# Kernel optimization log

Measured on AMD Instinct MI355X. Metric: run time of the kernel, lower is better.

Reference implementation:

```python
import jax, jax.numpy as jnp
import numpy as np

B, T, N, IN_DIM, H = 8, 16, 1024, 2, 128
HEADS, HD = 8, 16            # HEADS*HD == H (DGL GATConv head-concat)
SNP, SEQ_OUT, DEG = 4, 12, 8
NT = SNP * N                 # nodes per HSTG graph
CKPNT = [4, 7, 10, 13, 16]   # _generate_checkpoints(4, 16)
LRELU = 0.2


def _build_edges():
    # HSTG: per-snapshot spatial edges (random deg-8 adjacency + self-loops)
    # plus identity temporal edges t -> t+1 (uni-direction, non-dense, sync).
    rng = np.random.default_rng(0)
    src, dst = [], []
    ar = np.arange(N)
    for t in range(SNP):
        off = t * N
        src.append(rng.integers(0, N, size=N * DEG) + off)
        dst.append(np.repeat(ar, DEG) + off)
        src.append(ar + off)   # self-loops (keep every dst non-empty)
        dst.append(ar + off)
    for t in range(SNP - 1):
        src.append(ar + t * N)
        dst.append(ar + (t + 1) * N)
    return (jnp.asarray(np.concatenate(src), dtype=jnp.int32),
            jnp.asarray(np.concatenate(dst), dtype=jnp.int32))


def setup_inputs() -> dict:
    key = jax.random.key(0)
    ks = jax.random.split(key, 16)
    edge_src, edge_dst = _build_edges()
    rn = lambda k, s, sc: jax.random.normal(k, s, dtype=jnp.float32) * sc
    return {
        'inputs': rn(ks[0], (B, T, N, IN_DIM), 1.0),
        'W_in': rn(ks[1], (IN_DIM, H), 0.5),
        'b_in': jnp.zeros((H,), jnp.float32),
        'spatial_emb': rn(ks[2], (N, H), 0.05),
        'temporal_emb': rn(ks[3], (N, T), 0.05),
        'gat_w0': rn(ks[4], (H, HEADS * HD), 0.1),
        'gat_al0': rn(ks[5], (HEADS, HD), 0.1),
        'gat_ar0': rn(ks[6], (HEADS, HD), 0.1),
        'gat_b0': jnp.zeros((HEADS * HD,), jnp.float32),
        'gat_w1': rn(ks[7], (H, HEADS * HD), 0.1),
        'gat_al1': rn(ks[8], (HEADS, HD), 0.1),
        'gat_ar1': rn(ks[9], (HEADS, HD), 0.1),
        'gat_b1': jnp.zeros((HEADS * HD,), jnp.float32),
        'agg_q': rn(ks[10], (N, H), 0.1),
        'w_out1': rn(ks[11], (1, SEQ_OUT), 0.5),
        'b_out1': jnp.zeros((SEQ_OUT,), jnp.float32),
        'w_out2': rn(ks[12], (H, 1), 0.1),
        'b_out2': jnp.zeros((1,), jnp.float32),
        'edge_src': edge_src,
        'edge_dst': edge_dst,
    }


def _gat_layer(x, W, a_l, a_r, b, src, dst, activate):
    # x: [NT, H] node features of one graph
    feat = (x @ W).reshape(NT, HEADS, HD)
    el = jnp.sum(feat * a_l, axis=-1)                 # [NT, HEADS]
    er = jnp.sum(feat * a_r, axis=-1)
    e = jax.nn.leaky_relu(el[src] + er[dst], LRELU)    # [E, HEADS]
    m = jax.ops.segment_max(e, dst, num_segments=NT)
    w = jnp.exp(e - m[dst])
    s = jax.ops.segment_sum(w, dst, num_segments=NT)
    alpha = w / s[dst]
    out = jax.ops.segment_sum(feat[src] * alpha[..., None], dst, num_segments=NT)
    out = out.reshape(NT, HEADS * HD) + b
    return jax.nn.elu(out) if activate else out


def reference(inputs, W_in, b_in, spatial_emb, temporal_emb,
              gat_w0, gat_al0, gat_ar0, gat_b0,
              gat_w1, gat_al1, gat_ar1, gat_b1,
              agg_q, w_out1, b_out1, w_out2, b_out2,
              edge_src, edge_dst):
    # input projection + spatial/temporal embeddings
    x = inputs @ W_in + b_in                           # [B,T,N,H]
    x = x + spatial_emb                                # broadcast [N,H]
    x = x + temporal_emb.T[None, :, :, None]           # add temb[n,t] at [b,t,n,h]

    def gat(xb):  # xb: [NT,H], one sample of the batched block-diagonal graph
        h = _gat_layer(xb, gat_w0, gat_al0, gat_ar0, gat_b0, edge_src, edge_dst, True)
        return _gat_layer(h, gat_w1, gat_al1, gat_ar1, gat_b1, edge_src, edge_dst, False)
    gat_b = jax.vmap(gat)

    last = None
    left = 0
    for idx, right in enumerate(CKPNT):
        fs = x[:, left:right]                          # [B, snp or snp-1, N, H]
        if idx != 0:
            fs = jnp.concatenate([last, fs], axis=1)   # [B, SNP, N, H]
        residual = fs
        h = gat_b(fs.reshape(B, NT, H)).reshape(B, SNP, N, H)
        h = h + residual
        # Aggregator: per-node attention over the SNP snapshots -> [B,1,N,H]
        scores = jnp.einsum('btnh,nh->btn', h, agg_q)
        alpha = jax.nn.softmax(scores, axis=1)
        last = jnp.einsum('btn,btnh->bnh', alpha, h)[:, None]
        # LayerNorm over normalized_shape [1,N,H], no affine
        mu = jnp.mean(last, axis=(1, 2, 3), keepdims=True)
        var = jnp.var(last, axis=(1, 2, 3), keepdims=True)
        last = (last - mu) * jax.lax.rsqrt(var + 1e-5)
        left = right

    # decoder (meta_decode = False)
    t = jnp.transpose(last, (0, 3, 2, 1))              # [B,H,N,1]
    o = jax.nn.relu(t @ w_out1 + b_out1)               # [B,H,N,SEQ_OUT]
    o = jnp.transpose(o, (0, 3, 2, 1))                 # [B,SEQ_OUT,N,H]
    return o @ w_out2 + b_out2                         # [B,SEQ_OUT,N,1]
```

## Files before the change

### kernel.cpp

```cpp
#include <hip/hip_runtime.h>
#include <hip/hip_bf16.h>
#include <math.h>

constexpr int kB = 8;
constexpr int kT = 16;
constexpr int kN = 1024;
constexpr int kH = 128;
constexpr int kSNP = 4;
constexpr int kNT = kSNP * kN;
constexpr int kRows = kB * kNT;
constexpr int kSeqOut = 12;
constexpr float kLRelu = 0.2f;
constexpr int kEdgePerSnap = kN * 8 + kN;
constexpr int kSelfOff = kN * 8;
constexpr int kTempBase = kSNP * kEdgePerSnap;
constexpr int kStatsPerIter = kB * 16 * 16;

typedef __bf16 bf16x8 __attribute__((ext_vector_type(8)));
typedef float f32x4 __attribute__((ext_vector_type(4)));
typedef float f32x2 __attribute__((ext_vector_type(2)));

__device__ __forceinline__ f32x4 nt_load4(const float* p) {
  return __builtin_nontemporal_load((const f32x4*)p);
}
__device__ __forceinline__ void nt_store1(float* p, float v) {
  __builtin_nontemporal_store(v, p);
}
__device__ __forceinline__ void nt_store2(float* p, f32x2 v) {
  __builtin_nontemporal_store(v, (f32x2*)p);
}

__global__ void prep_w(const float* __restrict__ gw0, const float* __restrict__ gw1,
                       unsigned short* __restrict__ wbuf) {
  int tid = blockIdx.x * 256 + threadIdx.x;
  int layer = tid >> 14;
  int e = tid & 16383;
  int k = e >> 7, col = e & 127;
  const float* W = layer ? gw1 : gw0;
  float w = W[k * kH + col];
  unsigned int bits = __float_as_uint(w);
  unsigned short hi = (unsigned short)(bits >> 16);
  float hif = __uint_as_float(bits & 0xffff0000u);
  unsigned short lo = (unsigned short)(__float_as_uint(w - hif) >> 16);
  int s = k >> 5, q = (k >> 3) & 3, j = k & 7;
  int off = ((s * 4 + q) * kH + col) * 8 + j;
  wbuf[layer * 32768 + off] = hi;
  wbuf[layer * 32768 + 16384 + off] = lo;
}

template <int BUILD>
__launch_bounds__(256)
__global__ void gemm_mfma(const float* __restrict__ In,
                          const unsigned short* __restrict__ Wh,
                          const unsigned short* __restrict__ Wl,
                          const float* __restrict__ gal, const float* __restrict__ gar,
                          float* __restrict__ Out, float* __restrict__ elp,
                          float* __restrict__ erp,
                          const float* __restrict__ inputs, const float* __restrict__ W_in,
                          const float* __restrict__ b_in, const float* __restrict__ spatial,
                          const float* __restrict__ temporal, const float* __restrict__ last,
                          const float* __restrict__ stats, int left, int first) {
  __shared__ unsigned short AhL[64 * 128];
  __shared__ unsigned short AlL[64 * 128];
  int tid = threadIdx.x;
  int lane = tid & 63, wid = tid >> 6;
  int blk = blockIdx.x;
  int b = blk & 7;
  int inner = blk >> 3;
  int blockRow0 = (b << 12) + inner * 64;
  int colL = lane & 15;
  int q = lane >> 4;

  bf16x8 bh[2][4], bl[2][4];
  #pragma unroll
  for (int c = 0; c < 2; ++c) {
    int col = wid * 32 + c * 16 + colL;
    #pragma unroll
    for (int s = 0; s < 4; ++s) {
      int off = ((s * 4 + q) * kH + col) * 8;
      bh[c][s] = *(const bf16x8*)(Wh + off);
      bl[c][s] = *(const bf16x8*)(Wl + off);
    }
  }

  int tblk = inner >> 4;
  int nbase = (inner & 15) << 6;
  float mu = 0.f, scn = 0.f;
  bool lnpath = BUILD && !first && tblk == 0;
  if (lnpath) {
    float s1 = 0.f, s2 = 0.f;
    #pragma unroll
    for (int s = 0; s < 16; ++s) {
      s1 += stats[b * 256 + s * 16];
      s2 += stats[b * 256 + s * 16 + 1];
    }
    const float inv = 1.0f / (float)(kN * kH);
    mu = s1 * inv;
    float var = s2 * inv - mu * mu;
    scn = rsqrtf(var + 1e-5f);
  }
  const float* Ablk = In + (size_t)blockRow0 * kH;
  #pragma unroll
  for (int itn = 0; itn < 8; ++itn) {
    int fid = itn * 256 + tid;
    int row = fid >> 5, kq = fid & 31;
    f32x4 v;
    if (BUILD) {
      int n = nbase + row;
      if (lnpath) {
        const float* lp = last + ((size_t)(b * kN + n)) * kH + kq * 4;
        v[0] = (lp[0] - mu) * scn; v[1] = (lp[1] - mu) * scn;
        v[2] = (lp[2] - mu) * scn; v[3] = (lp[3] - mu) * scn;
      } else {
        int tg = left + tblk - (first ? 0 : 1);
        float2 iv = *(const float2*)(inputs + ((size_t)((b * kT + tg) * kN + n)) * 2);
        float tv = temporal[n * kT + tg];
        const float* w0 = W_in + kq * 4;
        const float* w1 = W_in + kH + kq * 4;
        const float* bb = b_in + kq * 4;
        const float* sp = spatial + (size_t)n * kH + kq * 4;
        #pragma unroll
        for (int j = 0; j < 4; ++j)
          v[j] = iv.x * w0[j] + iv.y * w1[j] + bb[j] + sp[j] + tv;
      }
    } else {
      v = nt_load4(Ablk + (size_t)row * kH + kq * 4);
    }
    ushort4 hi, lo;
    unsigned int bx = __float_as_uint(v[0]);
    hi.x = bx >> 16; lo.x = __float_as_uint(v[0] - __uint_as_float(bx & 0xffff0000u)) >> 16;
    unsigned int by = __float_as_uint(v[1]);
    hi.y = by >> 16; lo.y = __float_as_uint(v[1] - __uint_as_float(by & 0xffff0000u)) >> 16;
    unsigned int bz = __float_as_uint(v[2]);
    hi.z = bz >> 16; lo.z = __float_as_uint(v[2] - __uint_as_float(bz & 0xffff0000u)) >> 16;
    unsigned int bw = __float_as_uint(v[3]);
    hi.w = bw >> 16; lo.w = __float_as_uint(v[3] - __uint_as_float(bw & 0xffff0000u)) >> 16;
    int boff = (row * 256 + kq * 8) ^ ((row & 7) << 4);
    *(ushort4*)((char*)AhL + boff) = hi;
    *(ushort4*)((char*)AlL + boff) = lo;
  }
  __syncthreads();

  f32x4 acc[4][2];
  #pragma unroll
  for (int rb = 0; rb < 4; ++rb)
    #pragma unroll
    for (int c = 0; c < 2; ++c) acc[rb][c] = (f32x4){0.f, 0.f, 0.f, 0.f};

  #pragma unroll
  for (int s = 0; s < 4; ++s) {
    bf16x8 ah[4], alr[4];
    #pragma unroll
    for (int rb = 0; rb < 4; ++rb) {
      int row = rb * 16 + colL;
      int boff = (row * 256 + s * 64 + q * 16) ^ ((row & 7) << 4);
      ah[rb]  = *(const bf16x8*)((const char*)AhL + boff);
      alr[rb] = *(const bf16x8*)((const char*)AlL + boff);
    }
    #pragma unroll
    for (int c = 0; c < 2; ++c) {
      #pragma unroll
      for (int rb = 0; rb < 4; ++rb)
        acc[rb][c] = __builtin_amdgcn_mfma_f32_16x16x32_bf16(ah[rb], bh[c][s], acc[rb][c], 0, 0, 0);
      #pragma unroll
      for (int rb = 0; rb < 4; ++rb)
        acc[rb][c] = __builtin_amdgcn_mfma_f32_16x16x32_bf16(alr[rb], bh[c][s], acc[rb][c], 0, 0, 0);
      #pragma unroll
      for (int rb = 0; rb < 4; ++rb)
        acc[rb][c] = __builtin_amdgcn_mfma_f32_16x16x32_bf16(ah[rb], bl[c][s], acc[rb][c], 0, 0, 0);
    }
  }

  int rquad = q * 4;
  #pragma unroll
  for (int c = 0; c < 2; ++c) {
    int h = wid * 2 + c;
    float alv = gal[h * 16 + colL];
    float arv = gar[h * 16 + colL];
    int col = wid * 32 + c * 16 + colL;
    #pragma unroll
    for (int rb = 0; rb < 4; ++rb) {
      f32x4 a = acc[rb][c];
      int row0g = blockRow0 + rb * 16 + rquad;
      #pragma unroll
      for (int r = 0; r < 4; ++r)
        nt_store1(Out + (size_t)(row0g + r) * kH + col, a[r]);
      float e0 = a[0] * alv, e1 = a[1] * alv, e2 = a[2] * alv, e3 = a[3] * alv;
      float f0 = a[0] * arv, f1 = a[1] * arv, f2 = a[2] * arv, f3 = a[3] * arv;
      #pragma unroll
      for (int m = 1; m < 16; m <<= 1) {
        e0 += __shfl_xor(e0, m, 64); e1 += __shfl_xor(e1, m, 64);
        e2 += __shfl_xor(e2, m, 64); e3 += __shfl_xor(e3, m, 64);
        f0 += __shfl_xor(f0, m, 64); f1 += __shfl_xor(f1, m, 64);
        f2 += __shfl_xor(f2, m, 64); f3 += __shfl_xor(f3, m, 64);
      }
      if (colL == 0) {
        elp[(size_t)(row0g + 0) * 8 + h] = e0;
        elp[(size_t)(row0g + 1) * 8 + h] = e1;
        elp[(size_t)(row0g + 2) * 8 + h] = e2;
        elp[(size_t)(row0g + 3) * 8 + h] = e3;
        erp[(size_t)(row0g + 0) * 8 + h] = f0;
        erp[(size_t)(row0g + 1) * 8 + h] = f1;
        erp[(size_t)(row0g + 2) * 8 + h] = f2;
        erp[(size_t)(row0g + 3) * 8 + h] = f3;
      }
    }
  }
}

__launch_bounds__(256)
__global__ void agg0_kernel(const float* __restrict__ feat, const float* __restrict__ el,
                            const float* __restrict__ er, const int* __restrict__ esrc,
                            const float* __restrict__ bias, float* __restrict__ outp) {
  int blk = blockIdx.x;
  int b = blk & 7;
  int grp = blk >> 3;
  int tid = threadIdx.x;
  int wave = tid >> 6, lane = tid & 63;
  int v = grp * 4 + wave;
  int t = v >> 10, n = v & 1023;
  int h = lane >> 3;
  int bv = (b << 12) + v;

  int srcs[10];
  int base8 = t * kEdgePerSnap + n * 8;
  #pragma unroll
  for (int k = 0; k < 8; ++k) srcs[k] = esrc[base8 + k];
  srcs[8] = esrc[t * kEdgePerSnap + kSelfOff + n];
  float erv = er[bv * 8 + h];
  int ebase = b << 15;

  float e[10];
  float m = -1e30f;
  #pragma unroll
  for (int i = 0; i < 9; ++i) {
    float x = el[ebase + srcs[i] * 8 + h] + erv;
    x = x > 0.f ? x : kLRelu * x;
    e[i] = x;
    m = fmaxf(m, x);
  }
  if (t > 0) {
    int s9 = esrc[kTempBase + (t - 1) * kN + n];
    srcs[9] = s9;
    float x = el[ebase + s9 * 8 + h] + erv;
    x = x > 0.f ? x : kLRelu * x;
    e[9] = x;
    m = fmaxf(m, x);
  } else {
    srcs[9] = v;
    e[9] = -1e30f;
  }
  float s = 0.f;
  #pragma unroll
  for (int i = 0; i < 10; ++i) { e[i] = expf(e[i] - m); s += e[i]; }
  float inv = 1.0f / s;

  float ax = 0.f, ay = 0.f;
  size_t fbase = (size_t)(b << 12) * kH;
  #pragma unroll
  for (int i = 0; i < 10; ++i) {
    float w = e[i] * inv;
    float2 fv = *(const float2*)(feat + fbase + (size_t)srcs[i] * kH + lane * 2);
    ax += w * fv.x;
    ay += w * fv.y;
  }
  float2 bb = *(const float2*)(bias + lane * 2);
  float x0 = ax + bb.x, x1 = ay + bb.y;
  f32x2 o;
  o[0] = x0 > 0.f ? x0 : expm1f(x0);
  o[1] = x1 > 0.f ? x1 : expm1f(x1);
  nt_store2(outp + (size_t)bv * kH + lane * 2, o);
}

__launch_bounds__(256)
__global__ void agg1_attn(const float* __restrict__ feat, const float* __restrict__ el,
                          const float* __restrict__ er, const int* __restrict__ esrc,
                          const float* __restrict__ bias, const float* __restrict__ q,
                          float* __restrict__ last, float* __restrict__ stats,
                          const float* __restrict__ inputs, const float* __restrict__ W_in,
                          const float* __restrict__ b_in, const float* __restrict__ spatial,
                          const float* __restrict__ temporal,
                          const float* __restrict__ st_prev, int left, int first) {
  __shared__ float ssc[4];
  __shared__ float hbuf[4][128];
  __shared__ float sred[8];
  int blk = blockIdx.x;
  int b = blk & 7;
  int n = blk >> 3;
  int tid = threadIdx.x;
  int t = tid >> 6, lane = tid & 63;
  int v = (t << 10) + n;
  int h = lane >> 3;
  int bv = (b << 12) + v;

  int srcs[10];
  int base8 = t * kEdgePerSnap + n * 8;
  #pragma unroll
  for (int k = 0; k < 8; ++k) srcs[k] = esrc[base8 + k];
  srcs[8] = esrc[t * kEdgePerSnap + kSelfOff + n];
  float erv = er[bv * 8 + h];
  int ebase = b << 15;

  float e[10];
  float m = -1e30f;
  #pragma unroll
  for (int i = 0; i < 9; ++i) {
    float x = el[ebase + srcs[i] * 8 + h] + erv;
    x = x > 0.f ? x : kLRelu * x;
    e[i] = x;
    m = fmaxf(m, x);
  }
  if (t > 0) {
    int s9 = esrc[kTempBase + (t - 1) * kN + n];
    srcs[9] = s9;
    float x = el[ebase + s9 * 8 + h] + erv;
    x = x > 0.f ? x : kLRelu * x;
    e[9] = x;
    m = fmaxf(m, x);
  } else {
    srcs[9] = v;
    e[9] = -1e30f;
  }
  float s = 0.f;
  #pragma unroll
  for (int i = 0; i < 10; ++i) { e[i] = expf(e[i] - m); s += e[i]; }
  float inv = 1.0f / s;

  float ax = 0.f, ay = 0.f;
  size_t fbase = (size_t)(b << 12) * kH;
  #pragma unroll
  for (int i = 0; i < 10; ++i) {
    float w = e[i] * inv;
    float2 fv = *(const float2*)(feat + fbase + (size_t)srcs[i] * kH + lane * 2);
    ax += w * fv.x;
    ay += w * fv.y;
  }
  float2 bb = *(const float2*)(bias + lane * 2);

  int d0 = lane * 2;
  float rx, ry;
  if (!first && t == 0) {
    float s1 = 0.f, s2 = 0.f;
    #pragma unroll
    for (int ss = 0; ss < 16; ++ss) {
      s1 += st_prev[b * 256 + ss * 16];
      s2 += st_prev[b * 256 + ss * 16 + 1];
    }
    const float invq = 1.0f / (float)(kN * kH);
    float muq = s1 * invq;
    float varq = s2 * invq - muq * muq;
    float scq = rsqrtf(varq + 1e-5f);
    float2 lv = *(const float2*)(last + ((size_t)(b * kN + n)) * kH + d0);
    rx = (lv.x - muq) * scq;
    ry = (lv.y - muq) * scq;
  } else {
    int tg = left + t - (first ? 0 : 1);
    float2 iv = *(const float2*)(inputs + ((size_t)((b * kT + tg) * kN + n)) * 2);
    float tv = temporal[n * kT + tg];
    rx = iv.x * W_in[d0]     + iv.y * W_in[kH + d0]     + b_in[d0]     + spatial[(size_t)n * kH + d0]     + tv;
    ry = iv.x * W_in[d0 + 1] + iv.y * W_in[kH + d0 + 1] + b_in[d0 + 1] + spatial[(size_t)n * kH + d0 + 1] + tv;
  }
  float hx = ax + bb.x + rx;
  float hy = ay + bb.y + ry;

  float2 qv = *(const float2*)(q + (size_t)n * kH + d0);
  float p = hx * qv.x + hy * qv.y;
  #pragma unroll
  for (int s_ = 1; s_ < 64; s_ <<= 1) p += __shfl_xor(p, s_, 64);
  if (lane == 0) ssc[t] = p;
  __syncthreads();
  float s0 = ssc[0], s1 = ssc[1], s2 = ssc[2], s3 = ssc[3];
  float mm = fmaxf(fmaxf(s0, s1), fmaxf(s2, s3));
  float a0 = expf(s0 - mm), a1 = expf(s1 - mm), a2 = expf(s2 - mm), a3 = expf(s3 - mm);
  float denom = 1.0f / (a0 + a1 + a2 + a3);
  float at = (t == 0 ? a0 : t == 1 ? a1 : t == 2 ? a2 : a3) * denom;
  hbuf[t][d0]     = hx * at;
  hbuf[t][d0 + 1] = hy * at;
  __syncthreads();

  float p1 = 0.f, p2 = 0.f;
  if (tid < 128) {
    int d = tid;
    float sum = hbuf[0][d] + hbuf[1][d] + hbuf[2][d] + hbuf[3][d];
    last[((size_t)(b * kN + n)) * kH + d] = sum;
    p1 = sum;
    p2 = sum * sum;
  }
  #pragma unroll
  for (int s_ = 1; s_ < 64; s_ <<= 1) {
    p1 += __shfl_xor(p1, s_, 64);
    p2 += __shfl_xor(p2, s_, 64);
  }
  if (tid < 128 && lane == 0) { sred[t * 2] = p1; sred[t * 2 + 1] = p2; }
  __syncthreads();
  if (tid == 0) {
    int slot = n & 15;
    atomicAdd(&stats[b * 256 + slot * 16],     sred[0] + sred[2]);
    atomicAdd(&stats[b * 256 + slot * 16 + 1], sred[1] + sred[3]);
  }
}

__global__ void out_kernel(const float* __restrict__ last, const float* __restrict__ stats,
                           const float* __restrict__ w1, const float* __restrict__ b1,
                           const float* __restrict__ w2, const float* __restrict__ b2,
                           float* __restrict__ out) {
  int tid = threadIdx.x;
  int wave = tid >> 6, lane = tid & 63;
  int gw = blockIdx.x * 4 + wave;
  int b = gw >> 10, n = gw & 1023;
  float s1 = 0.f, s2 = 0.f;
  #pragma unroll
  for (int s = 0; s < 16; ++s) {
    s1 += stats[b * 256 + s * 16];
    s2 += stats[b * 256 + s * 16 + 1];
  }
  const float inv = 1.0f / (float)(kN * kH);
  float mu = s1 * inv;
  float var = s2 * inv - mu * mu;
  float scv = rsqrtf(var + 1e-5f);
  int d0 = lane * 2;
  float2 lv = *(const float2*)(last + ((size_t)(b * kN + n)) * kH + d0);
  float x0 = (lv.x - mu) * scv, x1 = (lv.y - mu) * scv;
  float w20 = w2[d0], w21 = w2[d0 + 1];
  float bias2 = b2[0];
  #pragma unroll
  for (int s = 0; s < kSeqOut; ++s) {
    float w1s = w1[s], b1s = b1[s];
    float v = fmaxf(x0 * w1s + b1s, 0.f) * w20 + fmaxf(x1 * w1s + b1s, 0.f) * w21;
    #pragma unroll
    for (int k = 1; k < 64; k <<= 1) v += __shfl_xor(v, k, 64);
    if (lane == 0) out[(size_t)(b * kSeqOut + s) * kN + n] = v + bias2;
  }
}

extern "C" void kernel_launch(void* const* d_in, const int* in_sizes, int n_in,
                              void* d_out, int out_size, void* d_ws, size_t ws_size,
                              hipStream_t stream) {
  const float* inputs   = (const float*)d_in[0];
  const float* W_in     = (const float*)d_in[1];
  const float* b_in     = (const float*)d_in[2];
  const float* spatial  = (const float*)d_in[3];
  const float* temporal = (const float*)d_in[4];
  const float* gw0      = (const float*)d_in[5];
  const float* gal0     = (const float*)d_in[6];
  const float* gar0     = (const float*)d_in[7];
  const float* gb0      = (const float*)d_in[8];
  const float* gw1      = (const float*)d_in[9];
  const float* gal1     = (const float*)d_in[10];
  const float* gar1     = (const float*)d_in[11];
  const float* gb1      = (const float*)d_in[12];
  const float* aggq     = (const float*)d_in[13];
  const float* w_out1   = (const float*)d_in[14];
  const float* b_out1   = (const float*)d_in[15];
  const float* w_out2   = (const float*)d_in[16];
  const float* b_out2   = (const float*)d_in[17];
  const int*   esrc     = (const int*)d_in[18];

  float* ws = (float*)d_ws;
  float* Bf    = ws;
  float* C     = ws + 4194304;
  float* el    = ws + 8388608;
  float* er    = ws + 8650752;
  float* last  = ws + 8912896;
  float* stats = ws + 9961472;
  unsigned short* wsplit = (unsigned short*)(ws + 9971712);

  hipMemsetAsync(stats, 0, 5 * kStatsPerIter * sizeof(float), stream);
  prep_w<<<128, 256, 0, stream>>>(gw0, gw1, wsplit);
  const unsigned short* w0h = wsplit;
  const unsigned short* w0l = wsplit + 16384;
  const unsigned short* w1h = wsplit + 32768;
  const unsigned short* w1l = wsplit + 49152;

  const int lefts[5] = {0, 4, 7, 10, 13};
  for (int it = 0; it < 5; ++it) {
    const float* st_prev = (it == 0) ? stats : (stats + (it - 1) * kStatsPerIter);
    int first = (it == 0) ? 1 : 0;
    gemm_mfma<1><<<kRows / 64, 256, 0, stream>>>(
        nullptr, w0h, w0l, gal0, gar0, Bf, el, er,
        inputs, W_in, b_in, spatial, temporal, last, st_prev, lefts[it], first);
    agg0_kernel<<<8192, 256, 0, stream>>>(Bf, el, er, esrc, gb0, C);
    gemm_mfma<0><<<kRows / 64, 256, 0, stream>>>(
        C, w1h, w1l, gal1, gar1, Bf, el, er,
        inputs, W_in, b_in, spatial, temporal, last, st_prev, 0, 1);
    agg1_attn<<<8192, 256, 0, stream>>>(Bf, el, er, esrc, gb1, aggq, last,
                                        stats + it * kStatsPerIter,
                                        inputs, W_in, b_in, spatial, temporal,
                                        st_prev, lefts[it], first);
  }
  out_kernel<<<2048, 256, 0, stream>>>(last, stats + 4 * kStatsPerIter, w_out1, b_out1,
                                       w_out2, b_out2, (float*)d_out);
}
```

Measured before the change: 517.2 us.

## Process four nodes per block in GAT aggregation kernels and drop nontemporal hints

Both aggregation kernels now loop over four nodes per block, with grids cut from 8192 to 2048 blocks and launch bounds raised to request 8 blocks per CU. In agg1_attn the LayerNorm statistics from the previous iteration are computed once per block instead of once per node. Nontemporal loads and stores in the GEMM and agg0 are replaced with ordinary cached accesses, so intermediates may stay in cache for the next kernel. The serial loop with #pragma unroll 1 gives up some latency hiding across nodes, and the block-level syncs in agg1 now repeat four times per block.

```diff
diff --git a/kernel.cpp b/kernel.cpp
--- a/kernel.cpp
+++ b/kernel.cpp
@@ -18,17 +18,6 @@
 
 typedef __bf16 bf16x8 __attribute__((ext_vector_type(8)));
 typedef float f32x4 __attribute__((ext_vector_type(4)));
-typedef float f32x2 __attribute__((ext_vector_type(2)));
-
-__device__ __forceinline__ f32x4 nt_load4(const float* p) {
-  return __builtin_nontemporal_load((const f32x4*)p);
-}
-__device__ __forceinline__ void nt_store1(float* p, float v) {
-  __builtin_nontemporal_store(v, p);
-}
-__device__ __forceinline__ void nt_store2(float* p, f32x2 v) {
-  __builtin_nontemporal_store(v, (f32x2*)p);
-}
 
 __global__ void prep_w(const float* __restrict__ gw0, const float* __restrict__ gw1,
                        unsigned short* __restrict__ wbuf) {
@@ -124,7 +113,7 @@
           v[j] = iv.x * w0[j] + iv.y * w1[j] + bb[j] + sp[j] + tv;
       }
     } else {
-      v = nt_load4(Ablk + (size_t)row * kH + kq * 4);
+      v = *(const f32x4*)(Ablk + (size_t)row * kH + kq * 4);
     }
     ushort4 hi, lo;
     unsigned int bx = __float_as_uint(v[0]);
@@ -184,7 +173,7 @@
       int row0g = blockRow0 + rb * 16 + rquad;
       #pragma unroll
       for (int r = 0; r < 4; ++r)
-        nt_store1(Out + (size_t)(row0g + r) * kH + col, a[r]);
+        Out[(size_t)(row0g + r) * kH + col] = a[r];
       float e0 = a[0] * alv, e1 = a[1] * alv, e2 = a[2] * alv, e3 = a[3] * alv;
       float f0 = a[0] * arv, f1 = a[1] * arv, f2 = a[2] * arv, f3 = a[3] * arv;
       #pragma unroll
@@ -208,71 +197,75 @@
   }
 }
 
-__launch_bounds__(256)
+__launch_bounds__(256, 8)
 __global__ void agg0_kernel(const float* __restrict__ feat, const float* __restrict__ el,
                             const float* __restrict__ er, const int* __restrict__ esrc,
                             const float* __restrict__ bias, float* __restrict__ outp) {
   int blk = blockIdx.x;
   int b = blk & 7;
-  int grp = blk >> 3;
+  int inner = blk >> 3;
   int tid = threadIdx.x;
   int wave = tid >> 6, lane = tid & 63;
-  int v = grp * 4 + wave;
-  int t = v >> 10, n = v & 1023;
   int h = lane >> 3;
-  int bv = (b << 12) + v;
-
-  int srcs[10];
-  int base8 = t * kEdgePerSnap + n * 8;
-  #pragma unroll
-  for (int k = 0; k < 8; ++k) srcs[k] = esrc[base8 + k];
-  srcs[8] = esrc[t * kEdgePerSnap + kSelfOff + n];
-  float erv = er[bv * 8 + h];
   int ebase = b << 15;
-
-  float e[10];
-  float m = -1e30f;
-  #pragma unroll
-  for (int i = 0; i < 9; ++i) {
-    float x = el[ebase + srcs[i] * 8 + h] + erv;
-    x = x > 0.f ? x : kLRelu * x;
-    e[i] = x;
-    m = fmaxf(m, x);
-  }
-  if (t > 0) {
-    int s9 = esrc[kTempBase + (t - 1) * kN + n];
-    srcs[9] = s9;
-    float x = el[ebase + s9 * 8 + h] + erv;
-    x = x > 0.f ? x : kLRelu * x;
-    e[9] = x;
-    m = fmaxf(m, x);
-  } else {
-    srcs[9] = v;
-    e[9] = -1e30f;
-  }
-  float s = 0.f;
-  #pragma unroll
-  for (int i = 0; i < 10; ++i) { e[i] = expf(e[i] - m); s += e[i]; }
-  float inv = 1.0f / s;
-
-  float ax = 0.f, ay = 0.f;
   size_t fbase = (size_t)(b << 12) * kH;
-  #pragma unroll
-  for (int i = 0; i < 10; ++i) {
-    float w = e[i] * inv;
-    float2 fv = *(const float2*)(feat + fbase + (size_t)srcs[i] * kH + lane * 2);
-    ax += w * fv.x;
-    ay += w * fv.y;
-  }
   float2 bb = *(const float2*)(bias + lane * 2);
-  float x0 = ax + bb.x, x1 = ay + bb.y;
-  f32x2 o;
-  o[0] = x0 > 0.f ? x0 : expm1f(x0);
-  o[1] = x1 > 0.f ? x1 : expm1f(x1);
-  nt_store2(outp + (size_t)bv * kH + lane * 2, o);
-}
-
-__launch_bounds__(256)
+
+  #pragma unroll 1
+  for (int it = 0; it < 4; ++it) {
+    int v = inner * 16 + it * 4 + wave;
+    int t = v >> 10, n = v & 1023;
+    int bv = (b << 12) + v;
+
+    int srcs[10];
+    int base8 = t * kEdgePerSnap + n * 8;
+    #pragma unroll
+    for (int k = 0; k < 8; ++k) srcs[k] = esrc[base8 + k];
+    srcs[8] = esrc[t * kEdgePerSnap + kSelfOff + n];
+    float erv = er[bv * 8 + h];
+
+    float e[10];
+    float m = -1e30f;
+    #pragma unroll
+    for (int i = 0; i < 9; ++i) {
+      float x = el[ebase + srcs[i] * 8 + h] + erv;
+      x = x > 0.f ? x : kLRelu * x;
+      e[i] = x;
+      m = fmaxf(m, x);
+    }
+    if (t > 0) {
+      int s9 = esrc[kTempBase + (t - 1) * kN + n];
+      srcs[9] = s9;
+      float x = el[ebase + s9 * 8 + h] + erv;
+      x = x > 0.f ? x : kLRelu * x;
+      e[9] = x;
+      m = fmaxf(m, x);
+    } else {
+      srcs[9] = v;
+      e[9] = -1e30f;
+    }
+    float s = 0.f;
+    #pragma unroll
+    for (int i = 0; i < 10; ++i) { e[i] = expf(e[i] - m); s += e[i]; }
+    float inv = 1.0f / s;
+
+    float ax = 0.f, ay = 0.f;
+    #pragma unroll
+    for (int i = 0; i < 10; ++i) {
+      float w = e[i] * inv;
+      float2 fv = *(const float2*)(feat + fbase + (size_t)srcs[i] * kH + lane * 2);
+      ax += w * fv.x;
+      ay += w * fv.y;
+    }
+    float x0 = ax + bb.x, x1 = ay + bb.y;
+    float2 o;
+    o.x = x0 > 0.f ? x0 : expm1f(x0);
+    o.y = x1 > 0.f ? x1 : expm1f(x1);
+    *(float2*)(outp + (size_t)bv * kH + lane * 2) = o;
+  }
+}
+
+__launch_bounds__(256, 8)
 __global__ void agg1_attn(const float* __restrict__ feat, const float* __restrict__ el,
                           const float* __restrict__ er, const int* __restrict__ esrc,
                           const float* __restrict__ bias, const float* __restrict__ q,
@@ -286,59 +279,16 @@
   __shared__ float sred[8];
   int blk = blockIdx.x;
   int b = blk & 7;
-  int n = blk >> 3;
+  int inner = blk >> 3;
   int tid = threadIdx.x;
   int t = tid >> 6, lane = tid & 63;
-  int v = (t << 10) + n;
   int h = lane >> 3;
-  int bv = (b << 12) + v;
-
-  int srcs[10];
-  int base8 = t * kEdgePerSnap + n * 8;
-  #pragma unroll
-  for (int k = 0; k < 8; ++k) srcs[k] = esrc[base8 + k];
-  srcs[8] = esrc[t * kEdgePerSnap + kSelfOff + n];
-  float erv = er[bv * 8 + h];
+  int d0 = lane * 2;
   int ebase = b << 15;
-
-  float e[10];
-  float m = -1e30f;
-  #pragma unroll
-  for (int i = 0; i < 9; ++i) {
-    float x = el[ebase + srcs[i] * 8 + h] + erv;
-    x = x > 0.f ? x : kLRelu * x;
-    e[i] = x;
-    m = fmaxf(m, x);
-  }
-  if (t > 0) {
-    int s9 = esrc[kTempBase + (t - 1) * kN + n];
-    srcs[9] = s9;
-    float x = el[ebase + s9 * 8 + h] + erv;
-    x = x > 0.f ? x : kLRelu * x;
-    e[9] = x;
-    m = fmaxf(m, x);
-  } else {
-    srcs[9] = v;
-    e[9] = -1e30f;
-  }
-  float s = 0.f;
-  #pragma unroll
-  for (int i = 0; i < 10; ++i) { e[i] = expf(e[i] - m); s += e[i]; }
-  float inv = 1.0f / s;
-
-  float ax = 0.f, ay = 0.f;
   size_t fbase = (size_t)(b << 12) * kH;
-  #pragma unroll
-  for (int i = 0; i < 10; ++i) {
-    float w = e[i] * inv;
-    float2 fv = *(const float2*)(feat + fbase + (size_t)srcs[i] * kH + lane * 2);
-    ax += w * fv.x;
-    ay += w * fv.y;
-  }
-  float2 bb = *(const float2*)(bias + lane * 2);
-
-  int d0 = lane * 2;
-  float rx, ry;
+  float2 bb = *(const float2*)(bias + d0);
+
+  float muq = 0.f, scq = 0.f;
   if (!first && t == 0) {
     float s1 = 0.f, s2 = 0.f;
     #pragma unroll
@@ -347,56 +297,108 @@
       s2 += st_prev[b * 256 + ss * 16 + 1];
     }
     const float invq = 1.0f / (float)(kN * kH);
-    float muq = s1 * invq;
+    muq = s1 * invq;
     float varq = s2 * invq - muq * muq;
-    float scq = rsqrtf(varq + 1e-5f);
-    float2 lv = *(const float2*)(last + ((size_t)(b * kN + n)) * kH + d0);
-    rx = (lv.x - muq) * scq;
-    ry = (lv.y - muq) * scq;
-  } else {
-    int tg = left + t - (first ? 0 : 1);
-    float2 iv = *(const float2*)(inputs + ((size_t)((b * kT + tg) * kN + n)) * 2);
-    float tv = temporal[n * kT + tg];
-    rx = iv.x * W_in[d0]     + iv.y * W_in[kH + d0]     + b_in[d0]     + spatial[(size_t)n * kH + d0]     + tv;
-    ry = iv.x * W_in[d0 + 1] + iv.y * W_in[kH + d0 + 1] + b_in[d0 + 1] + spatial[(size_t)n * kH + d0 + 1] + tv;
-  }
-  float hx = ax + bb.x + rx;
-  float hy = ay + bb.y + ry;
-
-  float2 qv = *(const float2*)(q + (size_t)n * kH + d0);
-  float p = hx * qv.x + hy * qv.y;
-  #pragma unroll
-  for (int s_ = 1; s_ < 64; s_ <<= 1) p += __shfl_xor(p, s_, 64);
-  if (lane == 0) ssc[t] = p;
-  __syncthreads();
-  float s0 = ssc[0], s1 = ssc[1], s2 = ssc[2], s3 = ssc[3];
-  float mm = fmaxf(fmaxf(s0, s1), fmaxf(s2, s3));
-  float a0 = expf(s0 - mm), a1 = expf(s1 - mm), a2 = expf(s2 - mm), a3 = expf(s3 - mm);
-  float denom = 1.0f / (a0 + a1 + a2 + a3);
-  float at = (t == 0 ? a0 : t == 1 ? a1 : t == 2 ? a2 : a3) * denom;
-  hbuf[t][d0]     = hx * at;
-  hbuf[t][d0 + 1] = hy * at;
-  __syncthreads();
-
-  float p1 = 0.f, p2 = 0.f;
-  if (tid < 128) {
-    int d = tid;
-    float sum = hbuf[0][d] + hbuf[1][d] + hbuf[2][d] + hbuf[3][d];
-    last[((size_t)(b * kN + n)) * kH + d] = sum;
-    p1 = sum;
-    p2 = sum * sum;
-  }
-  #pragma unroll
-  for (int s_ = 1; s_ < 64; s_ <<= 1) {
-    p1 += __shfl_xor(p1, s_, 64);
-    p2 += __shfl_xor(p2, s_, 64);
-  }
-  if (tid < 128 && lane == 0) { sred[t * 2] = p1; sred[t * 2 + 1] = p2; }
-  __syncthreads();
-  if (tid == 0) {
-    int slot = n & 15;
-    atomicAdd(&stats[b * 256 + slot * 16],     sred[0] + sred[2]);
-    atomicAdd(&stats[b * 256 + slot * 16 + 1], sred[1] + sred[3]);
+    scq = rsqrtf(varq + 1e-5f);
+  }
+
+  #pragma unroll 1
+  for (int i4 = 0; i4 < 4; ++i4) {
+    int n = inner * 4 + i4;
+    int v = (t << 10) + n;
+    int bv = (b << 12) + v;
+
+    int srcs[10];
+    int base8 = t * kEdgePerSnap + n * 8;
+    #pragma unroll
+    for (int k = 0; k < 8; ++k) srcs[k] = esrc[base8 + k];
+    srcs[8] = esrc[t * kEdgePerSnap + kSelfOff + n];
+    float erv = er[bv * 8 + h];
+
+    float e[10];
+    float m = -1e30f;
+    #pragma unroll
+    for (int i = 0; i < 9; ++i) {
+      float x = el[ebase + srcs[i] * 8 + h] + erv;
+      x = x > 0.f ? x : kLRelu * x;
+      e[i] = x;
+      m = fmaxf(m, x);
+    }
+    if (t > 0) {
+      int s9 = esrc[kTempBase + (t - 1) * kN + n];
+      srcs[9] = s9;
+      float x = el[ebase + s9 * 8 + h] + erv;
+      x = x > 0.f ? x : kLRelu * x;
+      e[9] = x;
+      m = fmaxf(m, x);
+    } else {
+      srcs[9] = v;
+      e[9] = -1e30f;
+    }
+    float s = 0.f;
+    #pragma unroll
+    for (int i = 0; i < 10; ++i) { e[i] = expf(e[i] - m); s += e[i]; }
+    float inv = 1.0f / s;
+
+    float ax = 0.f, ay = 0.f;
+    #pragma unroll
+    for (int i = 0; i < 10; ++i) {
+      float w = e[i] * inv;
+      float2 fv = *(const float2*)(feat + fbase + (size_t)srcs[i] * kH + d0);
+      ax += w * fv.x;
+      ay += w * fv.y;
+    }
+
+    float rx, ry;
+    if (!first && t == 0) {
+      float2 lv = *(const float2*)(last + ((size_t)(b * kN + n)) * kH + d0);
+      rx = (lv.x - muq) * scq;
+      ry = (lv.y - muq) * scq;
+    } else {
+      int tg = left + t - (first ? 0 : 1);
+      float2 iv = *(const float2*)(inputs + ((size_t)((b * kT + tg) * kN + n)) * 2);
+      float tv = temporal[n * kT + tg];
+      rx = iv.x * W_in[d0]     + iv.y * W_in[kH + d0]     + b_in[d0]     + spatial[(size_t)n * kH + d0]     + tv;
+      ry = iv.x * W_in[d0 + 1] + iv.y * W_in[kH + d0 + 1] + b_in[d0 + 1] + spatial[(size_t)n * kH + d0 + 1] + tv;
+    }
+    float hx = ax + bb.x + rx;
+    float hy = ay + bb.y + ry;
+
+    float2 qv = *(const float2*)(q + (size_t)n * kH + d0);
+    float p = hx * qv.x + hy * qv.y;
+    #pragma unroll
+    for (int s_ = 1; s_ < 64; s_ <<= 1) p += __shfl_xor(p, s_, 64);
+    if (lane == 0) ssc[t] = p;
+    __syncthreads();
+    float s0 = ssc[0], s1 = ssc[1], s2 = ssc[2], s3 = ssc[3];
+    float mm = fmaxf(fmaxf(s0, s1), fmaxf(s2, s3));
+    float a0 = expf(s0 - mm), a1 = expf(s1 - mm), a2 = expf(s2 - mm), a3 = expf(s3 - mm);
+    float denom = 1.0f / (a0 + a1 + a2 + a3);
+    float at = (t == 0 ? a0 : t == 1 ? a1 : t == 2 ? a2 : a3) * denom;
+    hbuf[t][d0]     = hx * at;
+    hbuf[t][d0 + 1] = hy * at;
+    __syncthreads();
+
+    float p1 = 0.f, p2 = 0.f;
+    if (tid < 128) {
+      int d = tid;
+      float sum = hbuf[0][d] + hbuf[1][d] + hbuf[2][d] + hbuf[3][d];
+      last[((size_t)(b * kN + n)) * kH + d] = sum;
+      p1 = sum;
+      p2 = sum * sum;
+    }
+    #pragma unroll
+    for (int s_ = 1; s_ < 64; s_ <<= 1) {
+      p1 += __shfl_xor(p1, s_, 64);
+      p2 += __shfl_xor(p2, s_, 64);
+    }
+    if (tid < 128 && lane == 0) { sred[t * 2] = p1; sred[t * 2 + 1] = p2; }
+    __syncthreads();
+    if (tid == 0) {
+      int slot = n & 15;
+      atomicAdd(&stats[b * 256 + slot * 16],     sred[0] + sred[2]);
+      atomicAdd(&stats[b * 256 + slot * 16 + 1], sred[1] + sred[3]);
+    }
   }
 }
 
@@ -479,11 +481,11 @@
     gemm_mfma<1><<<kRows / 64, 256, 0, stream>>>(
         nullptr, w0h, w0l, gal0, gar0, Bf, el, er,
         inputs, W_in, b_in, spatial, temporal, last, st_prev, lefts[it], first);
-    agg0_kernel<<<8192, 256, 0, stream>>>(Bf, el, er, esrc, gb0, C);
+    agg0_kernel<<<2048, 256, 0, stream>>>(Bf, el, er, esrc, gb0, C);
     gemm_mfma<0><<<kRows / 64, 256, 0, stream>>>(
         C, w1h, w1l, gal1, gar1, Bf, el, er,
         inputs, W_in, b_in, spatial, temporal, last, st_prev, 0, 1);
-    agg1_attn<<<8192, 256, 0, stream>>>(Bf, el, er, esrc, gb1, aggq, last,
+    agg1_attn<<<2048, 256, 0, stream>>>(Bf, el, er, esrc, gb1, aggq, last,
                                         stats + it * kStatsPerIter,
                                         inputs, W_in, b_in, spatial, temporal,
                                         st_prev, lefts[it], first);
```

New measurement: 608.4 us. 17.6% more time.

## Store GAT projected features in bf16 and prefetch neighbor gathers early

Applied to the files above, without the earlier changes.

The GEMM epilogue now writes the projected node features as round-to-nearest bf16 instead of fp32, which halves the intermediate buffer and the gather traffic in both aggregation kernels. The aggregation kernels issue all ten neighbor feature loads up front, before the attention softmax, so memory latency overlaps the score computation. Nontemporal load and store hints are replaced with plain accesses. The cost is reduced precision in the aggregated features, while the attention logits stay fp32, plus scattered 2-byte stores from the GEMM epilogue.

```diff
diff --git a/kernel.cpp b/kernel.cpp
--- a/kernel.cpp
+++ b/kernel.cpp
@@ -18,16 +18,14 @@
 
 typedef __bf16 bf16x8 __attribute__((ext_vector_type(8)));
 typedef float f32x4 __attribute__((ext_vector_type(4)));
-typedef float f32x2 __attribute__((ext_vector_type(2)));
-
-__device__ __forceinline__ f32x4 nt_load4(const float* p) {
-  return __builtin_nontemporal_load((const f32x4*)p);
-}
-__device__ __forceinline__ void nt_store1(float* p, float v) {
-  __builtin_nontemporal_store(v, p);
-}
-__device__ __forceinline__ void nt_store2(float* p, f32x2 v) {
-  __builtin_nontemporal_store(v, (f32x2*)p);
+
+__device__ __forceinline__ unsigned short f2bf_rn(float x) {
+  unsigned int b = __float_as_uint(x);
+  unsigned int r = b + 0x7FFFu + ((b >> 16) & 1u);
+  return (unsigned short)(r >> 16);
+}
+__device__ __forceinline__ float bf2f(unsigned short u) {
+  return __uint_as_float((unsigned int)u << 16);
 }
 
 __global__ void prep_w(const float* __restrict__ gw0, const float* __restrict__ gw1,
@@ -54,7 +52,7 @@
                           const unsigned short* __restrict__ Wh,
                           const unsigned short* __restrict__ Wl,
                           const float* __restrict__ gal, const float* __restrict__ gar,
-                          float* __restrict__ Out, float* __restrict__ elp,
+                          unsigned short* __restrict__ OutBf, float* __restrict__ elp,
                           float* __restrict__ erp,
                           const float* __restrict__ inputs, const float* __restrict__ W_in,
                           const float* __restrict__ b_in, const float* __restrict__ spatial,
@@ -124,7 +122,7 @@
           v[j] = iv.x * w0[j] + iv.y * w1[j] + bb[j] + sp[j] + tv;
       }
     } else {
-      v = nt_load4(Ablk + (size_t)row * kH + kq * 4);
+      v = *(const f32x4*)(Ablk + (size_t)row * kH + kq * 4);
     }
     ushort4 hi, lo;
     unsigned int bx = __float_as_uint(v[0]);
@@ -184,7 +182,7 @@
       int row0g = blockRow0 + rb * 16 + rquad;
       #pragma unroll
       for (int r = 0; r < 4; ++r)
-        nt_store1(Out + (size_t)(row0g + r) * kH + col, a[r]);
+        OutBf[(size_t)(row0g + r) * kH + col] = f2bf_rn(a[r]);
       float e0 = a[0] * alv, e1 = a[1] * alv, e2 = a[2] * alv, e3 = a[3] * alv;
       float f0 = a[0] * arv, f1 = a[1] * arv, f2 = a[2] * arv, f3 = a[3] * arv;
       #pragma unroll
@@ -209,7 +207,8 @@
 }
 
 __launch_bounds__(256)
-__global__ void agg0_kernel(const float* __restrict__ feat, const float* __restrict__ el,
+__global__ void agg0_kernel(const unsigned short* __restrict__ feat,
+                            const float* __restrict__ el,
                             const float* __restrict__ er, const int* __restrict__ esrc,
                             const float* __restrict__ bias, float* __restrict__ outp) {
   int blk = blockIdx.x;
@@ -227,9 +226,16 @@
   #pragma unroll
   for (int k = 0; k < 8; ++k) srcs[k] = esrc[base8 + k];
   srcs[8] = esrc[t * kEdgePerSnap + kSelfOff + n];
+  srcs[9] = (t > 0) ? esrc[kTempBase + (t - 1) * kN + n] : v;
+
+  size_t fbase = (size_t)(b << 12) * kH;
+  ushort2 fv[10];
+  #pragma unroll
+  for (int i = 0; i < 10; ++i)
+    fv[i] = *(const ushort2*)(feat + fbase + (size_t)srcs[i] * kH + lane * 2);
+
   float erv = er[bv * 8 + h];
   int ebase = b << 15;
-
   float e[10];
   float m = -1e30f;
   #pragma unroll
@@ -240,14 +246,11 @@
     m = fmaxf(m, x);
   }
   if (t > 0) {
-    int s9 = esrc[kTempBase + (t - 1) * kN + n];
-    srcs[9] = s9;
-    float x = el[ebase + s9 * 8 + h] + erv;
+    float x = el[ebase + srcs[9] * 8 + h] + erv;
     x = x > 0.f ? x : kLRelu * x;
     e[9] = x;
     m = fmaxf(m, x);
   } else {
-    srcs[9] = v;
     e[9] = -1e30f;
   }
   float s = 0.f;
@@ -256,24 +259,23 @@
   float inv = 1.0f / s;
 
   float ax = 0.f, ay = 0.f;
-  size_t fbase = (size_t)(b << 12) * kH;
   #pragma unroll
   for (int i = 0; i < 10; ++i) {
     float w = e[i] * inv;
-    float2 fv = *(const float2*)(feat + fbase + (size_t)srcs[i] * kH + lane * 2);
-    ax += w * fv.x;
-    ay += w * fv.y;
+    ax += w * bf2f(fv[i].x);
+    ay += w * bf2f(fv[i].y);
   }
   float2 bb = *(const float2*)(bias + lane * 2);
   float x0 = ax + bb.x, x1 = ay + bb.y;
-  f32x2 o;
-  o[0] = x0 > 0.f ? x0 : expm1f(x0);
-  o[1] = x1 > 0.f ? x1 : expm1f(x1);
-  nt_store2(outp + (size_t)bv * kH + lane * 2, o);
+  float2 o;
+  o.x = x0 > 0.f ? x0 : expm1f(x0);
+  o.y = x1 > 0.f ? x1 : expm1f(x1);
+  *(float2*)(outp + (size_t)bv * kH + lane * 2) = o;
 }
 
 __launch_bounds__(256)
-__global__ void agg1_attn(const float* __restrict__ feat, const float* __restrict__ el,
+__global__ void agg1_attn(const unsigned short* __restrict__ feat,
+                          const float* __restrict__ el,
                           const float* __restrict__ er, const int* __restrict__ esrc,
                           const float* __restrict__ bias, const float* __restrict__ q,
                           float* __restrict__ last, float* __restrict__ stats,
@@ -291,6 +293,7 @@
   int t = tid >> 6, lane = tid & 63;
   int v = (t << 10) + n;
   int h = lane >> 3;
+  int d0 = lane * 2;
   int bv = (b << 12) + v;
 
   int srcs[10];
@@ -298,9 +301,16 @@
   #pragma unroll
   for (int k = 0; k < 8; ++k) srcs[k] = esrc[base8 + k];
   srcs[8] = esrc[t * kEdgePerSnap + kSelfOff + n];
+  srcs[9] = (t > 0) ? esrc[kTempBase + (t - 1) * kN + n] : v;
+
+  size_t fbase = (size_t)(b << 12) * kH;
+  ushort2 fv[10];
+  #pragma unroll
+  for (int i = 0; i < 10; ++i)
+    fv[i] = *(const ushort2*)(feat + fbase + (size_t)srcs[i] * kH + d0);
+
   float erv = er[bv * 8 + h];
   int ebase = b << 15;
-
   float e[10];
   float m = -1e30f;
   #pragma unroll
@@ -311,14 +321,11 @@
     m = fmaxf(m, x);
   }
   if (t > 0) {
-    int s9 = esrc[kTempBase + (t - 1) * kN + n];
-    srcs[9] = s9;
-    float x = el[ebase + s9 * 8 + h] + erv;
+    float x = el[ebase + srcs[9] * 8 + h] + erv;
     x = x > 0.f ? x : kLRelu * x;
     e[9] = x;
     m = fmaxf(m, x);
   } else {
-    srcs[9] = v;
     e[9] = -1e30f;
   }
   float s = 0.f;
@@ -327,17 +334,14 @@
   float inv = 1.0f / s;
 
   float ax = 0.f, ay = 0.f;
-  size_t fbase = (size_t)(b << 12) * kH;
   #pragma unroll
   for (int i = 0; i < 10; ++i) {
     float w = e[i] * inv;
-    float2 fv = *(const float2*)(feat + fbase + (size_t)srcs[i] * kH + lane * 2);
-    ax += w * fv.x;
-    ay += w * fv.y;
-  }
-  float2 bb = *(const float2*)(bias + lane * 2);
-
-  int d0 = lane * 2;
+    ax += w * bf2f(fv[i].x);
+    ay += w * bf2f(fv[i].y);
+  }
+  float2 bb = *(const float2*)(bias + d0);
+
   float rx, ry;
   if (!first && t == 0) {
     float s1 = 0.f, s2 = 0.f;
@@ -457,13 +461,13 @@
   const int*   esrc     = (const int*)d_in[18];
 
   float* ws = (float*)d_ws;
-  float* Bf    = ws;
-  float* C     = ws + 4194304;
-  float* el    = ws + 8388608;
-  float* er    = ws + 8650752;
-  float* last  = ws + 8912896;
-  float* stats = ws + 9961472;
-  unsigned short* wsplit = (unsigned short*)(ws + 9971712);
+  unsigned short* BfU = (unsigned short*)ws;
+  float* C     = ws + 2097152;
+  float* el    = ws + 6291456;
+  float* er    = ws + 6553600;
+  float* last  = ws + 6815744;
+  float* stats = ws + 7864320;
+  unsigned short* wsplit = (unsigned short*)(ws + 7874560);
 
   hipMemsetAsync(stats, 0, 5 * kStatsPerIter * sizeof(float), stream);
   prep_w<<<128, 256, 0, stream>>>(gw0, gw1, wsplit);
@@ -477,13 +481,13 @@
     const float* st_prev = (it == 0) ? stats : (stats + (it - 1) * kStatsPerIter);
     int first = (it == 0) ? 1 : 0;
     gemm_mfma<1><<<kRows / 64, 256, 0, stream>>>(
-        nullptr, w0h, w0l, gal0, gar0, Bf, el, er,
+        nullptr, w0h, w0l, gal0, gar0, BfU, el, er,
         inputs, W_in, b_in, spatial, temporal, last, st_prev, lefts[it], first);
-    agg0_kernel<<<8192, 256, 0, stream>>>(Bf, el, er, esrc, gb0, C);
+    agg0_kernel<<<8192, 256, 0, stream>>>(BfU, el, er, esrc, gb0, C);
     gemm_mfma<0><<<kRows / 64, 256, 0, stream>>>(
-        C, w1h, w1l, gal1, gar1, Bf, el, er,
+        C, w1h, w1l, gal1, gar1, BfU, el, er,
         inputs, W_in, b_in, spatial, temporal, last, st_prev, 0, 1);
-    agg1_attn<<<8192, 256, 0, stream>>>(Bf, el, er, esrc, gb1, aggq, last,
+    agg1_attn<<<8192, 256, 0, stream>>>(BfU, el, er, esrc, gb1, aggq, last,
                                         stats + it * kStatsPerIter,
                                         inputs, W_in, b_in, spatial, temporal,
                                         st_prev, lefts[it], first);
```

After: 517.4 us. No clear change (+0.0%).
